# Kernel tuning notes

Measured on AMD Instinct MI355X. Metric: run time of the kernel, lower is better.

Reference implementation:

```python
import jax, jax.numpy as jnp
import numpy as np

N_NODES = 50000
N_EDGES = 800000
HEADS = 4
OUT_CH = 32
EDGE_EMB = 4
NEG_SLOPE = 0.2


def setup_inputs() -> dict:
    key = jax.random.key(0)
    ks = jax.random.split(key, 6)
    x = jax.random.normal(ks[0], (N_NODES, 128), dtype=jnp.float32)
    edge_index = jax.random.randint(ks[1], (2, N_EDGES), 0, N_NODES, dtype=jnp.int32)
    edge_attr = jax.random.normal(ks[2], (N_EDGES, 8), dtype=jnp.float32)
    W = jax.random.normal(ks[3], (128, HEADS * OUT_CH), dtype=jnp.float32) * 0.08
    We = jax.random.normal(ks[4], (8, HEADS * EDGE_EMB), dtype=jnp.float32) * 0.3
    att = jax.random.normal(ks[5], (1, HEADS, 2 * OUT_CH + EDGE_EMB), dtype=jnp.float32) * 0.1
    bias = jnp.zeros((HEADS * OUT_CH,), dtype=jnp.float32)
    return {"x": x, "edge_index": edge_index, "edge_attr": edge_attr,
            "W": W, "We": We, "att": att, "bias": bias}


def reference(x, edge_index, edge_attr, W, We, att, bias):
    # x: [N, Din], edge_index: [2, E] (row 0 = source j, row 1 = target i)
    src = edge_index[0]
    dst = edge_index[1]
    n = x.shape[0]

    xh = (x @ W).reshape(n, HEADS, OUT_CH)                    # [N, H, O]
    eh = (edge_attr @ We).reshape(-1, HEADS, EDGE_EMB)        # [E, H, P]

    a_i = att[0, :, :OUT_CH]                                  # [H, O]
    a_j = att[0, :, OUT_CH:2 * OUT_CH]                        # [H, O]
    a_e = att[0, :, 2 * OUT_CH:]                              # [H, P]

    # per-node dot with att halves, then gather per edge (avoids [E,H,O] concat)
    s_i = jnp.einsum('nho,ho->nh', xh, a_i)                   # [N, H]
    s_j = jnp.einsum('nho,ho->nh', xh, a_j)                   # [N, H]
    s_e = jnp.einsum('ehp,hp->eh', eh, a_e)                   # [E, H]

    alpha = s_i[dst] + s_j[src] + s_e                         # [E, H]
    alpha = jax.nn.leaky_relu(alpha, NEG_SLOPE)

    # segment softmax over incoming edges of each target node
    m = jax.ops.segment_max(alpha, dst, num_segments=n)       # [N, H]
    m = jnp.where(jnp.isfinite(m), m, 0.0)
    ea = jnp.exp(alpha - m[dst])                              # [E, H]
    denom = jax.ops.segment_sum(ea, dst, num_segments=n)      # [N, H]
    alpha = ea / (denom[dst] + 1e-16)                         # [E, H]

    msg = xh[src] * alpha[:, :, None]                         # [E, H, O]
    aggr = jax.ops.segment_sum(msg, dst, num_segments=n)      # [N, H, O]
    out = aggr.reshape(n, HEADS * OUT_CH) + bias              # concat heads
    return out
```

## Files before the change

kernel.cpp:

```cpp
#include <hip/hip_runtime.h>
#include <hip/hip_fp16.h>
#include <stdint.h>
#include <math.h>

#define NEG_SLOPE 0.2f

static __device__ __forceinline__ unsigned short f2bf(float f) {
    unsigned u = __float_as_uint(f);
    unsigned r = (u + 0x7FFFu + ((u >> 16) & 1u)) >> 16;
    return (unsigned short)r;
}
static __device__ __forceinline__ unsigned pack_h2(float a, float b) {
    __half2 h = __floats2half2_rn(a, b);
    return *(unsigned*)&h;
}

__global__ __launch_bounds__(256, 4) void k_gemm_scatter(
    const float* __restrict__ x, const float* __restrict__ W,
    const float* __restrict__ att, unsigned short* __restrict__ xh16,
    float* __restrict__ s_i, float* __restrict__ s_j, int n, int GB,
    const int* __restrict__ ei, const float* __restrict__ edge_attr,
    const float* __restrict__ We, int* __restrict__ cnt, int4* __restrict__ bucket,
    int slots, int E) {
    if (blockIdx.x >= GB) {
        __shared__ float ceS[32];
        int t = threadIdx.x;
        if (t < 32) {
            int k = t >> 2, h = t & 3;
            float s = 0.f;
            #pragma unroll
            for (int p = 0; p < 4; ++p)
                s += We[k * 16 + h * 4 + p] * att[h * 68 + 64 + p];
            ceS[t] = s;
        }
        __syncthreads();
        int e = (blockIdx.x - GB) * 256 + t;
        if (e < E) {
            float4 ea0 = *(const float4*)(edge_attr + (size_t)e * 8);
            float4 ea1 = *(const float4*)(edge_attr + (size_t)e * 8 + 4);
            float eav[8] = {ea0.x, ea0.y, ea0.z, ea0.w, ea1.x, ea1.y, ea1.z, ea1.w};
            float se[4];
            #pragma unroll
            for (int h = 0; h < 4; ++h) {
                float s = 0.f;
                #pragma unroll
                for (int k = 0; k < 8; ++k) s += eav[k] * ceS[k * 4 + h];
                se[h] = s;
            }
            int src = ei[e], dst = ei[E + e];
            int4 ent;
            ent.x = src;
            ent.y = (int)pack_h2(se[0], se[1]);
            ent.z = (int)pack_h2(se[2], se[3]);
            ent.w = 0;
            int p = atomicAdd(&cnt[dst], 1);
            if (p < slots) bucket[(size_t)dst * slots + p] = ent;
        }
        return;
    }
    __shared__ float wS[32 * 128];
    __shared__ float xS[64 * 32];
    int t = threadIdx.x;
    int c4 = t & 31;
    int rg = t >> 5;
    int r0 = blockIdx.x * 64;

    float acc[8][4];
    #pragma unroll
    for (int r = 0; r < 8; ++r)
        #pragma unroll
        for (int j = 0; j < 4; ++j) acc[r][j] = 0.f;

    for (int ch = 0; ch < 4; ++ch) {
        {
            const float4* Wv = (const float4*)(W + (size_t)ch * 32 * 128);
            #pragma unroll
            for (int i = 0; i < 4; ++i)
                ((float4*)wS)[t + i * 256] = Wv[t + i * 256];
        }
        #pragma unroll
        for (int i = 0; i < 2; ++i) {
            int idx = t + i * 256;
            int r = idx >> 3;
            int q = idx & 7;
            int row = r0 + r;
            float4 v = make_float4(0.f, 0.f, 0.f, 0.f);
            if (row < n) v = *(const float4*)(x + (size_t)row * 128 + ch * 32 + q * 4);
            ((float4*)xS)[idx] = v;
        }
        __syncthreads();
        #pragma unroll 1
        for (int q = 0; q < 8; ++q) {
            float4 wv0 = *(const float4*)&wS[(4 * q + 0) * 128 + 4 * c4];
            float4 wv1 = *(const float4*)&wS[(4 * q + 1) * 128 + 4 * c4];
            float4 wv2 = *(const float4*)&wS[(4 * q + 2) * 128 + 4 * c4];
            float4 wv3 = *(const float4*)&wS[(4 * q + 3) * 128 + 4 * c4];
            #pragma unroll
            for (int r = 0; r < 8; ++r) {
                float4 xv = ((const float4*)xS)[(rg * 8 + r) * 8 + q];
                acc[r][0] += xv.x * wv0.x + xv.y * wv1.x + xv.z * wv2.x + xv.w * wv3.x;
                acc[r][1] += xv.x * wv0.y + xv.y * wv1.y + xv.z * wv2.y + xv.w * wv3.y;
                acc[r][2] += xv.x * wv0.z + xv.y * wv1.z + xv.z * wv2.z + xv.w * wv3.z;
                acc[r][3] += xv.x * wv0.w + xv.y * wv1.w + xv.z * wv2.w + xv.w * wv3.w;
            }
        }
        __syncthreads();
    }

    int h = c4 >> 3;
    int cb = 4 * (c4 & 7);
    float ai[4], aj[4];
    #pragma unroll
    for (int j = 0; j < 4; ++j) {
        ai[j] = att[h * 68 + cb + j];
        aj[j] = att[h * 68 + 32 + cb + j];
    }
    #pragma unroll 1
    for (int r = 0; r < 8; ++r) {
        int row = r0 + rg * 8 + r;
        bool ok = row < n;
        if (ok) {
            ushort4 us;
            us.x = f2bf(acc[r][0]);
            us.y = f2bf(acc[r][1]);
            us.z = f2bf(acc[r][2]);
            us.w = f2bf(acc[r][3]);
            *(ushort4*)(xh16 + (size_t)row * 128 + 4 * c4) = us;
        }
        float pi = acc[r][0] * ai[0] + acc[r][1] * ai[1]
                 + acc[r][2] * ai[2] + acc[r][3] * ai[3];
        float pj = acc[r][0] * aj[0] + acc[r][1] * aj[1]
                 + acc[r][2] * aj[2] + acc[r][3] * aj[3];
        #pragma unroll
        for (int m = 1; m < 8; m <<= 1) {
            pi += __shfl_xor(pi, m);
            pj += __shfl_xor(pj, m);
        }
        if ((c4 & 7) == 0 && ok) {
            s_i[(size_t)row * 4 + h] = pi;
            s_j[(size_t)row * 4 + h] = pj;
        }
    }
}

__global__ __launch_bounds__(256) void k_aggr(
    const int* __restrict__ cnt, const int4* __restrict__ bucket, int slots,
    const float* __restrict__ s_i, const float* __restrict__ s_j,
    const unsigned* __restrict__ xh32, const float* __restrict__ bias,
    float* __restrict__ out, int n) {
    __shared__ float wbuf[4][64][4];
    __shared__ int sbuf[4][64];
    int wid = threadIdx.x >> 6;
    int l = threadIdx.x & 63;
    int node = blockIdx.x * 4 + wid;
    if (node >= n) return;
    int deg = cnt[node];
    deg = deg < slots ? deg : slots;
    float2 b = ((const float2*)bias)[l];
    float2* op = (float2*)(out + (size_t)node * 128);
    if (deg == 0) { op[l] = b; return; }

    float4 si4 = *(const float4*)(s_i + (size_t)node * 4);
    float lg[4];
    int src = 0;
    bool valid = l < deg;
    if (valid) {
        int4 ent = bucket[(size_t)node * slots + l];
        src = ent.x;
        float4 sj4 = *(const float4*)(s_j + (size_t)src * 4);
        __half2 se01 = *(__half2*)&ent.y;
        __half2 se23 = *(__half2*)&ent.z;
        float2 se01f = __half22float2(se01);
        float2 se23f = __half22float2(se23);
        float a;
        a = si4.x + sj4.x + se01f.x; lg[0] = a > 0.f ? a : NEG_SLOPE * a;
        a = si4.y + sj4.y + se01f.y; lg[1] = a > 0.f ? a : NEG_SLOPE * a;
        a = si4.z + sj4.z + se23f.x; lg[2] = a > 0.f ? a : NEG_SLOPE * a;
        a = si4.w + sj4.w + se23f.y; lg[3] = a > 0.f ? a : NEG_SLOPE * a;
    } else {
        lg[0] = lg[1] = lg[2] = lg[3] = -INFINITY;
    }
    float mx[4];
    #pragma unroll
    for (int h = 0; h < 4; ++h) mx[h] = lg[h];
    #pragma unroll
    for (int m = 1; m < 64; m <<= 1)
        #pragma unroll
        for (int h = 0; h < 4; ++h) mx[h] = fmaxf(mx[h], __shfl_xor(mx[h], m));
    float w[4], sm[4];
    #pragma unroll
    for (int h = 0; h < 4; ++h) {
        w[h] = valid ? __expf(lg[h] - mx[h]) : 0.f;
        sm[h] = w[h];
    }
    #pragma unroll
    for (int m = 1; m < 64; m <<= 1)
        #pragma unroll
        for (int h = 0; h < 4; ++h) sm[h] += __shfl_xor(sm[h], m);
    #pragma unroll
    for (int h = 0; h < 4; ++h) w[h] *= 1.f / (sm[h] + 1e-16f);

    *(float4*)&wbuf[wid][l][0] = make_float4(w[0], w[1], w[2], w[3]);
    sbuf[wid][l] = src;

    int hsel = l >> 4;
    float a0 = 0.f, a1 = 0.f;
    for (int j0 = 0; j0 < deg; j0 += 8) {
        int srcs[8];
        float ws[8];
        #pragma unroll
        for (int j = 0; j < 8; ++j) {
            int jj = j0 + j < deg ? j0 + j : 0;
            bool in = j0 + j < deg;
            srcs[j] = sbuf[wid][jj];
            ws[j] = in ? wbuf[wid][jj][hsel] : 0.f;
        }
        unsigned u[8];
        #pragma unroll
        for (int j = 0; j < 8; ++j) u[j] = xh32[(size_t)srcs[j] * 64 + l];
        #pragma unroll
        for (int j = 0; j < 8; ++j) {
            a0 += ws[j] * __uint_as_float(u[j] << 16);
            a1 += ws[j] * __uint_as_float(u[j] & 0xffff0000u);
        }
    }
    op[l] = make_float2(a0 + b.x, a1 + b.y);
}

extern "C" void kernel_launch(void* const* d_in, const int* in_sizes, int n_in,
                              void* d_out, int out_size, void* d_ws, size_t ws_size,
                              hipStream_t stream) {
    const float* x    = (const float*)d_in[0];
    const int*   ei   = (const int*)d_in[1];
    const float* eattr= (const float*)d_in[2];
    const float* W    = (const float*)d_in[3];
    const float* We   = (const float*)d_in[4];
    const float* att  = (const float*)d_in[5];
    const float* bias = (const float*)d_in[6];
    float* out = (float*)d_out;
    int n = in_sizes[0] / 128;
    int E = in_sizes[1] / 2;

    char* w = (char*)d_ws;
    auto alloc = [&](size_t bytes) {
        char* p = w;
        w += (bytes + 255) & ~(size_t)255;
        return (void*)p;
    };
    unsigned short* xh16 = (unsigned short*)alloc((size_t)n * 128 * 2);
    float* s_i           = (float*)alloc((size_t)n * 16);
    float* s_j           = (float*)alloc((size_t)n * 16);
    int* cnt             = (int*)alloc((size_t)n * 4);
    size_t remain = (ws_size > (size_t)(w - (char*)d_ws))
                  ? ws_size - (size_t)(w - (char*)d_ws) : 0;
    int slots = (int)(remain / ((size_t)n * 16));
    if (slots > 64) slots = 64;
    if (slots < 32) slots = 32;
    int4* bucket         = (int4*)alloc((size_t)n * slots * 16);

    int GB = (n + 63) / 64;
    int EB = (E + 255) / 256;

    (void)hipMemsetAsync(cnt, 0, (size_t)n * 4, stream);
    k_gemm_scatter<<<GB + EB, 256, 0, stream>>>(x, W, att, xh16, s_i, s_j, n, GB,
                                                ei, eattr, We, cnt, bucket, slots, E);
    k_aggr<<<(n + 3) / 4, 256, 0, stream>>>(cnt, bucket, slots, s_i, s_j,
                                            (const unsigned*)xh16, bias, out, n);
}
```

Measured before the change: 190.1 us.

## Split wave into two half-waves processing alternate edges with 8-byte gathers

The aggregation loop now has each half-wave (32 lanes) load 8 bytes (four bf16 features) per source row and handle alternate edges. Each iteration therefore covers 16 edges instead of 8, and the two partial sums are combined with a cross-half shuffle. The softmax max and sum reductions also skip the last two shuffle stages when the degree is at most 16. The aim is more memory-level parallelism per wave and fewer loop trips and shuffles, at the cost of an extra shuffle reduction and half the lanes sitting idle on the store.

```diff
diff --git a/kernel.cpp b/kernel.cpp
--- a/kernel.cpp
+++ b/kernel.cpp
@@ -156,9 +156,14 @@
     if (node >= n) return;
     int deg = cnt[node];
     deg = deg < slots ? deg : slots;
-    float2 b = ((const float2*)bias)[l];
-    float2* op = (float2*)(out + (size_t)node * 128);
-    if (deg == 0) { op[l] = b; return; }
+    int c = l & 31;
+    if (deg == 0) {
+        if (l < 32) {
+            float4 b4 = ((const float4*)bias)[c];
+            *(float4*)(out + (size_t)node * 128 + c * 4) = b4;
+        }
+        return;
+    }
 
     float4 si4 = *(const float4*)(s_i + (size_t)node * 4);
     float lg[4];
@@ -184,9 +189,15 @@
     #pragma unroll
     for (int h = 0; h < 4; ++h) mx[h] = lg[h];
     #pragma unroll
-    for (int m = 1; m < 64; m <<= 1)
+    for (int m = 1; m < 16; m <<= 1)
         #pragma unroll
         for (int h = 0; h < 4; ++h) mx[h] = fmaxf(mx[h], __shfl_xor(mx[h], m));
+    if (deg > 16) {
+        #pragma unroll
+        for (int m = 16; m < 64; m <<= 1)
+            #pragma unroll
+            for (int h = 0; h < 4; ++h) mx[h] = fmaxf(mx[h], __shfl_xor(mx[h], m));
+    }
     float w[4], sm[4];
     #pragma unroll
     for (int h = 0; h < 4; ++h) {
@@ -194,37 +205,56 @@
         sm[h] = w[h];
     }
     #pragma unroll
-    for (int m = 1; m < 64; m <<= 1)
+    for (int m = 1; m < 16; m <<= 1)
         #pragma unroll
         for (int h = 0; h < 4; ++h) sm[h] += __shfl_xor(sm[h], m);
+    if (deg > 16) {
+        #pragma unroll
+        for (int m = 16; m < 64; m <<= 1)
+            #pragma unroll
+            for (int h = 0; h < 4; ++h) sm[h] += __shfl_xor(sm[h], m);
+    }
     #pragma unroll
     for (int h = 0; h < 4; ++h) w[h] *= 1.f / (sm[h] + 1e-16f);
 
     *(float4*)&wbuf[wid][l][0] = make_float4(w[0], w[1], w[2], w[3]);
     sbuf[wid][l] = src;
 
-    int hsel = l >> 4;
-    float a0 = 0.f, a1 = 0.f;
-    for (int j0 = 0; j0 < deg; j0 += 8) {
+    int p2 = l >> 5;
+    int hsel = c >> 3;
+    const uint2* xh64 = (const uint2*)xh32;
+    float a0 = 0.f, a1 = 0.f, a2 = 0.f, a3 = 0.f;
+    for (int j0 = 0; j0 < deg; j0 += 16) {
         int srcs[8];
         float ws[8];
         #pragma unroll
         for (int j = 0; j < 8; ++j) {
-            int jj = j0 + j < deg ? j0 + j : 0;
-            bool in = j0 + j < deg;
+            int jp = j0 + 2 * j + p2;
+            int jj = jp < deg ? jp : 0;
+            bool in = jp < deg;
             srcs[j] = sbuf[wid][jj];
             ws[j] = in ? wbuf[wid][jj][hsel] : 0.f;
         }
-        unsigned u[8];
-        #pragma unroll
-        for (int j = 0; j < 8; ++j) u[j] = xh32[(size_t)srcs[j] * 64 + l];
+        uint2 u[8];
+        #pragma unroll
+        for (int j = 0; j < 8; ++j) u[j] = xh64[(size_t)srcs[j] * 32 + c];
         #pragma unroll
         for (int j = 0; j < 8; ++j) {
-            a0 += ws[j] * __uint_as_float(u[j] << 16);
-            a1 += ws[j] * __uint_as_float(u[j] & 0xffff0000u);
-        }
-    }
-    op[l] = make_float2(a0 + b.x, a1 + b.y);
+            a0 += ws[j] * __uint_as_float(u[j].x << 16);
+            a1 += ws[j] * __uint_as_float(u[j].x & 0xffff0000u);
+            a2 += ws[j] * __uint_as_float(u[j].y << 16);
+            a3 += ws[j] * __uint_as_float(u[j].y & 0xffff0000u);
+        }
+    }
+    a0 += __shfl_xor(a0, 32);
+    a1 += __shfl_xor(a1, 32);
+    a2 += __shfl_xor(a2, 32);
+    a3 += __shfl_xor(a3, 32);
+    if (l < 32) {
+        float4 b4 = ((const float4*)bias)[c];
+        *(float4*)(out + (size_t)node * 128 + c * 4) =
+            make_float4(a0 + b4.x, a1 + b4.y, a2 + b4.z, a3 + b4.w);
+    }
 }
 
 extern "C" void kernel_launch(void* const* d_in, const int* in_sizes, int n_in,
```

Result: no change. 189.3 us (-0.4%).
